# Optimization experiments

Measured on AMD Instinct MI355X. Metric: run time of the kernel, lower is better.

## Reference

```python
import jax, jax.numpy as jnp
import numpy as np

C = 256
INTER = C // 2


def _conv1x1(x, w, b):
    # x: [B,C,H,W], w: [O,C], b: [O] -> [B,O,H,W]
    return jnp.einsum('bchw,oc->bohw', x, w) + b[None, :, None, None]


def setup_inputs() -> dict:
    key = jax.random.key(0)
    ks = jax.random.split(key, 9)
    B, H, W = 4, 64, 64
    x = jax.random.normal(ks[0], (B, C, H, W), dtype=jnp.float32)
    s_in = 1.0 / np.sqrt(C)
    s_int = 1.0 / np.sqrt(INTER)
    return {
        'x': x,
        'w_g': jax.random.normal(ks[1], (INTER, C), jnp.float32) * s_in,
        'b_g': jax.random.normal(ks[2], (INTER,), jnp.float32) * 0.01,
        'w_theta': jax.random.normal(ks[3], (INTER, C), jnp.float32) * s_in,
        'b_theta': jax.random.normal(ks[4], (INTER,), jnp.float32) * 0.01,
        'w_phi': jax.random.normal(ks[5], (INTER, C), jnp.float32) * s_in,
        'b_phi': jax.random.normal(ks[6], (INTER,), jnp.float32) * 0.01,
        'w_W': jax.random.normal(ks[7], (C, INTER), jnp.float32) * s_int,
        'b_W': jax.random.normal(ks[8], (C,), jnp.float32) * 0.01,
    }


def reference(x, w_g, b_g, w_theta, b_theta, w_phi, b_phi, w_W, b_W):
    B, Cc, H, W = x.shape
    N = H * W
    # 1x1 conv projections -> flatten spatial to N
    g_x = _conv1x1(x, w_g, b_g).reshape(B, INTER, N).transpose(0, 2, 1)        # [B,N,I]
    theta_x = _conv1x1(x, w_theta, b_theta).reshape(B, INTER, N).transpose(0, 2, 1)  # [B,N,I]
    phi_x = _conv1x1(x, w_phi, b_phi).reshape(B, INTER, N)                     # [B,I,N]
    f = jnp.einsum('bni,bim->bnm', theta_x, phi_x)                             # [B,N,N]
    f_div_C = jax.nn.softmax(f, axis=-1)
    y = jnp.einsum('bnm,bmi->bni', f_div_C, g_x)                               # [B,N,I]
    y = y.transpose(0, 2, 1).reshape(B, INTER, H, W)
    W_y = _conv1x1(y, w_W, b_W)                                                # [B,C,H,W]
    return W_y + x
```

## Files before the change

### kernel.cpp

```cpp
#include <hip/hip_runtime.h>

typedef unsigned short ushort_t;
typedef unsigned int uint_t;
typedef _Float16 f16;
typedef __attribute__((ext_vector_type(8))) _Float16 f16x8;
typedef __attribute__((ext_vector_type(2))) _Float16 f16x2;
typedef __attribute__((ext_vector_type(4))) float f32x4;

#define B_ 4
#define C_ 256
#define I_ 128
#define N_ 4096
#define KVB 32
#define TOT_IT (N_ / KVB)
#define LOG2E 1.44269504f

#define W_F  0ull
#define TH_F 131072ull
#define PH_F 2228224ull
#define G3_F 4325376ull
#define YP_F 6422528ull

__device__ __forceinline__ float exp2_hw(float x) { return __builtin_amdgcn_exp2f(x); }
__device__ __forceinline__ float log2_hw(float x) { return __builtin_amdgcn_logf(x); }

__device__ __forceinline__ f16x2 pkrtz(float a, float b) {
    auto r = __builtin_amdgcn_cvt_pkrtz(a, b);
    f16x2 o;
    __builtin_memcpy(&o, &r, sizeof(o));
    return o;
}
__device__ __forceinline__ f32x4 mfma16h(f16x8 a, f16x8 b, f32x4 c) {
    return __builtin_amdgcn_mfma_f32_16x16x32_f16(a, b, c, 0, 0, 0);
}
__device__ __forceinline__ f32x4 zero4() { f32x4 z = {0.f, 0.f, 0.f, 0.f}; return z; }
__device__ __forceinline__ void gload_lds16(const void* g, void* lds) {
    __builtin_amdgcn_global_load_lds(
        (const __attribute__((address_space(1))) void*)g,
        (__attribute__((address_space(3))) void*)lds, 16, 0, 0);
}

__global__ __launch_bounds__(256) void k_convert_w(const float* wg, const float* wt,
                                                   const float* wp, const float* wW,
                                                   ushort_t* ws) {
    int idx = (blockIdx.x * 256 + threadIdx.x) * 16;
    const float* src;
    int off;
    if (idx < 32768)      { src = wg; off = idx; }
    else if (idx < 65536) { src = wt; off = idx - 32768; }
    else if (idx < 98304) { src = wp; off = idx - 65536; }
    else                  { src = wW; off = idx - 98304; }
    f16 o[16];
#pragma unroll
    for (int j = 0; j < 16; ++j) o[j] = (f16)src[off + j];
    f16* wd = (f16*)(ws + W_F);
    *(uint4*)&wd[idx]     = *(uint4*)&o[0];
    *(uint4*)&wd[idx + 8] = *(uint4*)&o[8];
}

__global__ __launch_bounds__(512) void k_projx(const float* x, const float* bg,
        const float* bth, const float* bph, ushort_t* ws) {
    __shared__ float t[64][65];
    __shared__ __align__(16) f16 xt[64][280];
    int b = blockIdx.y, n0 = blockIdx.x * 64;
    int tid = threadIdx.x;

    for (int q = 0; q < 4; ++q) {
        int c0 = q * 64;
#pragma unroll
        for (int p = 0; p < 2; ++p) {
            int row = p * 32 + (tid >> 4);
            int col4 = (tid & 15) * 4;
            float4 v = *(const float4*)(x + ((size_t)(b * C_ + c0 + row)) * N_ + n0 + col4);
            t[row][col4 + 0] = v.x; t[row][col4 + 1] = v.y;
            t[row][col4 + 2] = v.z; t[row][col4 + 3] = v.w;
        }
        __syncthreads();
        {
            int nl = tid & 63, cg = tid >> 6;
            f16 hv[8];
#pragma unroll
            for (int k = 0; k < 8; ++k) hv[k] = (f16)t[cg * 8 + k][nl];
            *(uint4*)&xt[nl][c0 + cg * 8] = *(uint4*)&hv[0];
        }
        __syncthreads();
    }

    int w = tid >> 6, l = tid & 63;
    int li = l & 15, lg = l >> 4;
    int wn = (w & 3) * 16;
    int ihb = (w >> 2) * 4;
    const f16* wf = (const f16*)(ws + W_F);

    f32x4 acc[3][4];
#pragma unroll
    for (int p = 0; p < 3; ++p)
#pragma unroll
        for (int t2 = 0; t2 < 4; ++t2) acc[p][t2] = zero4();

#pragma unroll 2
    for (int kb = 0; kb < 8; ++kb) {
        int kc = kb * 32 + 8 * lg;
        f16x8 ah = *(const f16x8*)&xt[wn + li][kc];
#pragma unroll
        for (int p = 0; p < 3; ++p)
#pragma unroll
            for (int t2 = 0; t2 < 4; ++t2) {
                f16x8 bw = *(const f16x8*)&wf[(size_t)p * 32768
                               + (size_t)((ihb + t2) * 16 + li) * C_ + kc];
                acc[p][t2] = mfma16h(ah, bw, acc[p][t2]);
            }
    }
    f16* g3p = (f16*)(ws + G3_F);
    f16* thp = (f16*)(ws + TH_F);
    f16* php = (f16*)(ws + PH_F);
#pragma unroll
    for (int p = 0; p < 3; ++p) {
        const float* bias = (p == 0) ? bg : (p == 1) ? bth : bph;
#pragma unroll
        for (int t2 = 0; t2 < 4; ++t2) {
            int i = (ihb + t2) * 16 + li;
            float bs = bias[i];
#pragma unroll
            for (int r = 0; r < 4; ++r) {
                int n = n0 + wn + 4 * lg + r;
                float v = acc[p][t2][r] + bs;
                if (p == 0) {
                    int tq = (n >> 2) & 3;
                    size_t gi = ((size_t)b * (N_ / 32) + (n >> 5)) * 4096
                              + (size_t)(tq * 128 + (i ^ (tq << 1))) * 8
                              + ((n >> 4) & 1) * 4 + (n & 3);
                    g3p[gi] = (f16)v;
                } else if (p == 1)
                    thp[((size_t)b * N_ + n) * I_ + i] = (f16)(v * LOG2E);
                else
                    php[((size_t)b * N_ + n) * I_ + i] = (f16)v;
            }
        }
    }
}

__global__ __launch_bounds__(256, 3) void k_attn(ushort_t* ws, float* lse, int splits) {
    __shared__ __align__(16) ushort_t smem[16384];
    int b = blockIdx.y, sp = blockIdx.z;
    int w = threadIdx.x >> 6, l = threadIdx.x & 63;
    int li = l & 15, lg = l >> 4;
    int q0 = blockIdx.x * 128 + w * 16;
    const f16* th = (const f16*)(ws + TH_F);
    const f16* ph = (const f16*)(ws + PH_F);
    const f16* g3 = (const f16*)(ws + G3_F);
    f16* yp = (f16*)(ws + YP_F) + (size_t)sp * 2097152ull;
    const f16* smf = (const f16*)smem;

    f16x8 qA[4], qB[4];
#pragma unroll
    for (int kb = 0; kb < 4; ++kb) {
        qA[kb] = *(const f16x8*)&th[((size_t)b * N_ + q0 + li) * I_ + kb * 32 + 8 * lg];
        qB[kb] = *(const f16x8*)&th[((size_t)b * N_ + q0 + 64 + li) * I_ + kb * 32 + 8 * lg];
    }

    int phOff[8];
#pragma unroll
    for (int kb = 0; kb < 4; ++kb) {
        int cc = ((kb * 4 + lg) ^ (li & 7)) * 8;
        phOff[kb * 2 + 0] = li * 128 + cc;
        phOff[kb * 2 + 1] = (16 + li) * 128 + cc;
    }
    int gBase = 8192 + (lg * 128 + (li ^ (lg << 1))) * 8;

    f32x4 yA[8], yB[8];
#pragma unroll
    for (int dt = 0; dt < 8; ++dt) { yA[dt] = zero4(); yB[dt] = zero4(); }
    float mA = -1e30f, lA = 0.f, mB = -1e30f, lB = 0.f;

    int beg = (sp * TOT_IT) / splits;
    int end = ((sp + 1) * TOT_IT) / splits;
    int nit = end - beg;
    int srow = l >> 4;
    const f16* srcP0 = ph + ((size_t)b * N_ + w * 8 + srow) * I_
                          + ((l & 15) ^ srow) * 8 + (size_t)beg * KVB * I_;
    const f16* srcP1 = ph + ((size_t)b * N_ + w * 8 + 4 + srow) * I_
                          + (((l & 15) ^ srow) ^ 4) * 8 + (size_t)beg * KVB * I_;
    const f16* srcG  = g3 + (size_t)b * (N_ / 32) * 4096 + w * 1024 + l * 8
                          + (size_t)beg * KVB * 128;

    gload_lds16(srcP0, smem + w * 1024);
    gload_lds16(srcP1, smem + w * 1024 + 512);
    gload_lds16(srcG,       smem + 8192 + w * 1024);
    gload_lds16(srcG + 512, smem + 8192 + w * 1024 + 512);
    srcP0 += 4096; srcP1 += 4096; srcG += 4096;
    __syncthreads();

#define ATTN_STEP(BUF, HASNEXT)                                                   \
    do {                                                                          \
        if (HASNEXT) {                                                            \
            gload_lds16(srcP0, smem + ((BUF) ^ 4096) + w * 1024);                 \
            gload_lds16(srcP1, smem + ((BUF) ^ 4096) + w * 1024 + 512);           \
            gload_lds16(srcG,       smem + 8192 + ((BUF) ^ 4096) + w * 1024);     \
            gload_lds16(srcG + 512, smem + 8192 + ((BUF) ^ 4096) + w * 1024 + 512);\
            srcP0 += 4096; srcP1 += 4096; srcG += 4096;                           \
        }                                                                         \
        f32x4 fA0 = zero4(), fA1 = zero4(), fB0 = zero4(), fB1 = zero4();         \
        __builtin_amdgcn_s_setprio(1);                                            \
        _Pragma("unroll")                                                         \
        for (int kb = 0; kb < 4; ++kb) {                                          \
            f16x8 a0 = *(const f16x8*)&smf[phOff[kb * 2 + 0] + (BUF)];            \
            f16x8 a1 = *(const f16x8*)&smf[phOff[kb * 2 + 1] + (BUF)];            \
            fA0 = mfma16h(a0, qA[kb], fA0);                                       \
            fB0 = mfma16h(a0, qB[kb], fB0);                                       \
            fA1 = mfma16h(a1, qA[kb], fA1);                                       \
            fB1 = mfma16h(a1, qB[kb], fB1);                                       \
        }                                                                         \
        __builtin_amdgcn_s_setprio(0);                                            \
        float tmA = fmaxf(fmaxf(fmaxf(fA0[0], fA0[1]), fmaxf(fA0[2], fA0[3])),    \
                          fmaxf(fmaxf(fA1[0], fA1[1]), fmaxf(fA1[2], fA1[3])));   \
        tmA = fmaxf(tmA, __shfl_xor(tmA, 16));                                    \
        tmA = fmaxf(tmA, __shfl_xor(tmA, 32));                                    \
        if (__ballot(tmA > mA + 11.0f)) {                                         \
            float mn = fmaxf(mA, tmA);                                            \
            float sc = exp2_hw(mA - mn);                                          \
            lA *= sc; mA = mn;                                                    \
            float s0 = __shfl(sc, 4 * lg + 0);                                    \
            float s1 = __shfl(sc, 4 * lg + 1);                                    \
            float s2 = __shfl(sc, 4 * lg + 2);                                    \
            float s3 = __shfl(sc, 4 * lg + 3);                                    \
            _Pragma("unroll")                                                     \
            for (int dt = 0; dt < 8; ++dt) {                                      \
                yA[dt][0] *= s0; yA[dt][1] *= s1;                                 \
                yA[dt][2] *= s2; yA[dt][3] *= s3;                                 \
            }                                                                     \
        }                                                                         \
        _Pragma("unroll")                                                         \
        for (int r = 0; r < 4; ++r) {                                             \
            fA0[r] = exp2_hw(fA0[r] - mA);                                        \
            fA1[r] = exp2_hw(fA1[r] - mA);                                        \
        }                                                                         \
        lA += ((fA0[0] + fA0[1]) + (fA0[2] + fA0[3]))                             \
            + ((fA1[0] + fA1[1]) + (fA1[2] + fA1[3]));                            \
        union PU { f16x2 h2[4]; f16x8 v; };                                       \
        PU pA, pB;                                                                \
        pA.h2[0] = pkrtz(fA0[0], fA0[1]); pA.h2[1] = pkrtz(fA0[2], fA0[3]);       \
        pA.h2[2] = pkrtz(fA1[0], fA1[1]); pA.h2[3] = pkrtz(fA1[2], fA1[3]);       \
        float tmB = fmaxf(fmaxf(fmaxf(fB0[0], fB0[1]), fmaxf(fB0[2], fB0[3])),    \
                          fmaxf(fmaxf(fB1[0], fB1[1]), fmaxf(fB1[2], fB1[3])));   \
        tmB = fmaxf(tmB, __shfl_xor(tmB, 16));                                    \
        tmB = fmaxf(tmB, __shfl_xor(tmB, 32));                                    \
        if (__ballot(tmB > mB + 11.0f)) {                                         \
            float mn = fmaxf(mB, tmB);                                            \
            float sc = exp2_hw(mB - mn);                                          \
            lB *= sc; mB = mn;                                                    \
            float s0 = __shfl(sc, 4 * lg + 0);                                    \
            float s1 = __shfl(sc, 4 * lg + 1);                                    \
            float s2 = __shfl(sc, 4 * lg + 2);                                    \
            float s3 = __shfl(sc, 4 * lg + 3);                                    \
            _Pragma("unroll")                                                     \
            for (int dt = 0; dt < 8; ++dt) {                                      \
                yB[dt][0] *= s0; yB[dt][1] *= s1;                                 \
                yB[dt][2] *= s2; yB[dt][3] *= s3;                                 \
            }                                                                     \
        }                                                                         \
        _Pragma("unroll")                                                         \
        for (int r = 0; r < 4; ++r) {                                             \
            fB0[r] = exp2_hw(fB0[r] - mB);                                        \
            fB1[r] = exp2_hw(fB1[r] - mB);                                        \
        }                                                                         \
        lB += ((fB0[0] + fB0[1]) + (fB0[2] + fB0[3]))                             \
            + ((fB1[0] + fB1[1]) + (fB1[2] + fB1[3]));                            \
        pB.h2[0] = pkrtz(fB0[0], fB0[1]); pB.h2[1] = pkrtz(fB0[2], fB0[3]);       \
        pB.h2[2] = pkrtz(fB1[0], fB1[1]); pB.h2[3] = pkrtz(fB1[2], fB1[3]);       \
        __builtin_amdgcn_s_setprio(1);                                            \
        _Pragma("unroll")                                                         \
        for (int dt = 0; dt < 8; ++dt) {                                          \
            f16x8 gv = *(const f16x8*)&smf[gBase + dt * 128 + (BUF)];             \
            yA[dt] = mfma16h(pA.v, gv, yA[dt]);                                   \
            yB[dt] = mfma16h(pB.v, gv, yB[dt]);                                   \
        }                                                                         \
        __builtin_amdgcn_s_setprio(0);                                            \
        __syncthreads();                                                          \
    } while (0)

    int it = 0;
    while (it + 2 <= nit) {
        ATTN_STEP(0, (it + 1 < nit));
        ATTN_STEP(4096, (it + 2 < nit));
        it += 2;
    }
    if (it < nit) ATTN_STEP(0, false);
#undef ATTN_STEP

    lA += __shfl_xor(lA, 16); lA += __shfl_xor(lA, 32);
    lB += __shfl_xor(lB, 16); lB += __shfl_xor(lB, 32);
    {
        float inv = 1.0f / lA;
        float i0 = __shfl(inv, 4 * lg + 0);
        float i1 = __shfl(inv, 4 * lg + 1);
        float i2 = __shfl(inv, 4 * lg + 2);
        float i3 = __shfl(inv, 4 * lg + 3);
#pragma unroll
        for (int dt = 0; dt < 8; ++dt) {
            size_t base = ((size_t)b * N_ + q0 + 4 * lg) * I_ + dt * 16 + li;
            yp[base]          = (f16)(yA[dt][0] * i0);
            yp[base + I_]     = (f16)(yA[dt][1] * i1);
            yp[base + 2 * I_] = (f16)(yA[dt][2] * i2);
            yp[base + 3 * I_] = (f16)(yA[dt][3] * i3);
        }
    }
    {
        float inv = 1.0f / lB;
        float i0 = __shfl(inv, 4 * lg + 0);
        float i1 = __shfl(inv, 4 * lg + 1);
        float i2 = __shfl(inv, 4 * lg + 2);
        float i3 = __shfl(inv, 4 * lg + 3);
#pragma unroll
        for (int dt = 0; dt < 8; ++dt) {
            size_t base = ((size_t)b * N_ + q0 + 64 + 4 * lg) * I_ + dt * 16 + li;
            yp[base]          = (f16)(yB[dt][0] * i0);
            yp[base + I_]     = (f16)(yB[dt][1] * i1);
            yp[base + 2 * I_] = (f16)(yB[dt][2] * i2);
            yp[base + 3 * I_] = (f16)(yB[dt][3] * i3);
        }
    }
    if (l < 16) {
        lse[((size_t)sp * B_ + b) * N_ + q0 + l]      = mA + log2_hw(lA);
        lse[((size_t)sp * B_ + b) * N_ + q0 + 64 + l] = mB + log2_hw(lB);
    }
}

__global__ __launch_bounds__(512) void k_out(const float* x, const float* bW,
        const ushort_t* ws, const float* lse, float* out, int splits) {
    __shared__ __align__(16) f16 ylds[64 * 136];
    int b = blockIdx.y, n0 = blockIdx.x * 64;
    int tid = threadIdx.x;
    {
        int nn = tid >> 3, ig = tid & 7;
        size_t lrow = (size_t)b * N_ + n0 + nn;
        float mx = -1e30f;
        for (int s = 0; s < splits; ++s)
            mx = fmaxf(mx, lse[(size_t)s * (B_ * N_) + lrow]);
        float sum = 0.f;
        for (int s = 0; s < splits; ++s)
            sum += exp2_hw(lse[(size_t)s * (B_ * N_) + lrow] - mx);
        float inv = 1.0f / sum;
        float acc[16];
#pragma unroll
        for (int j = 0; j < 16; ++j) acc[j] = 0.f;
        for (int s = 0; s < splits; ++s) {
            float wg = exp2_hw(lse[(size_t)s * (B_ * N_) + lrow] - mx) * inv;
            const f16* p = (const f16*)(ws + YP_F) + (size_t)s * 2097152ull
                         + lrow * I_ + ig * 16;
            f16x8 v0 = *(const f16x8*)p;
            f16x8 v1 = *(const f16x8*)(p + 8);
#pragma unroll
            for (int j = 0; j < 8; ++j) {
                acc[j]     += wg * (float)v0[j];
                acc[8 + j] += wg * (float)v1[j];
            }
        }
        f16 o[16];
#pragma unroll
        for (int j = 0; j < 16; ++j) o[j] = (f16)acc[j];
        *(uint4*)&ylds[nn * 136 + ig * 16]     = *(uint4*)&o[0];
        *(uint4*)&ylds[nn * 136 + ig * 16 + 8] = *(uint4*)&o[8];
    }
    __syncthreads();

    int w = tid >> 6, l = tid & 63;
    int li = l & 15, lg = l >> 4;
    int cw = (w >> 1) * 64, nh = (w & 1) * 32;
    const f16* wfp = (const f16*)(ws + W_F) + 98304;

    f32x4 acc2[4][2];
#pragma unroll
    for (int mm = 0; mm < 4; ++mm)
#pragma unroll
        for (int n = 0; n < 2; ++n) acc2[mm][n] = zero4();

#pragma unroll 2
    for (int kb = 0; kb < 4; ++kb) {
        int kc = kb * 32 + 8 * lg;
        f16x8 a[4], byv[2];
#pragma unroll
        for (int mm = 0; mm < 4; ++mm)
            a[mm] = *(const f16x8*)&wfp[(size_t)(cw + mm * 16 + li) * I_ + kc];
#pragma unroll
        for (int n = 0; n < 2; ++n)
            byv[n] = *(const f16x8*)&ylds[(nh + n * 16 + li) * 136 + kc];
#pragma unroll
        for (int mm = 0; mm < 4; ++mm)
#pragma unroll
            for (int n = 0; n < 2; ++n)
                acc2[mm][n] = mfma16h(a[mm], byv[n], acc2[mm][n]);
    }
#pragma unroll
    for (int mm = 0; mm < 4; ++mm)
#pragma unroll
        for (int n = 0; n < 2; ++n)
#pragma unroll
            for (int r = 0; r < 4; ++r) {
                int c = cw + mm * 16 + lg * 4 + r;
                int nn = n0 + nh + n * 16 + li;
                size_t xi = ((size_t)b * C_ + c) * N_ + nn;
                out[xi] = acc2[mm][n][r] + bW[c] + x[xi];
            }
}

extern "C" void kernel_launch(void* const* d_in, const int* in_sizes, int n_in,
                              void* d_out, int out_size, void* d_ws, size_t ws_size,
                              hipStream_t stream) {
    const float* x  = (const float*)d_in[0];
    const float* wg = (const float*)d_in[1];
    const float* bg = (const float*)d_in[2];
    const float* wt = (const float*)d_in[3];
    const float* bt = (const float*)d_in[4];
    const float* wp = (const float*)d_in[5];
    const float* bp = (const float*)d_in[6];
    const float* wW = (const float*)d_in[7];
    const float* bW = (const float*)d_in[8];
    ushort_t* ws = (ushort_t*)d_ws;
    float* out = (float*)d_out;

    int splits = (ws_size >= 46923776ull) ? 8
               : (ws_size >= 42663936ull) ? 7
               : (ws_size >= 38404096ull) ? 6 : 4;
    size_t lse_off = 2ull * (YP_F + (size_t)splits * 2097152ull);
    float* lse = (float*)((char*)d_ws + lse_off);

    k_convert_w<<<32, 256, 0, stream>>>(wg, wt, wp, wW, ws);
    k_projx<<<dim3(64, 4), 512, 0, stream>>>(x, bg, bt, bp, ws);
    k_attn<<<dim3(32, 4, splits), 256, 0, stream>>>(ws, lse, splits);
    k_out<<<dim3(64, 4), 512, 0, stream>>>(x, bW, ws, lse, out, splits);
}
```

Measured before the change: 104.7 us.

## Double block size of projection and output kernels, defer max shuffles in attention

```diff
diff --git a/kernel.cpp b/kernel.cpp
--- a/kernel.cpp
+++ b/kernel.cpp
@@ -58,7 +58,7 @@
     *(uint4*)&wd[idx + 8] = *(uint4*)&o[8];
 }
 
-__global__ __launch_bounds__(512) void k_projx(const float* x, const float* bg,
+__global__ __launch_bounds__(1024) void k_projx(const float* x, const float* bg,
         const float* bth, const float* bph, ushort_t* ws) {
     __shared__ float t[64][65];
     __shared__ __align__(16) f16 xt[64][280];
@@ -67,9 +67,8 @@
 
     for (int q = 0; q < 4; ++q) {
         int c0 = q * 64;
-#pragma unroll
-        for (int p = 0; p < 2; ++p) {
-            int row = p * 32 + (tid >> 4);
+        {
+            int row = tid >> 4;
             int col4 = (tid & 15) * 4;
             float4 v = *(const float4*)(x + ((size_t)(b * C_ + c0 + row)) * N_ + n0 + col4);
             t[row][col4 + 0] = v.x; t[row][col4 + 1] = v.y;
@@ -78,10 +77,10 @@
         __syncthreads();
         {
             int nl = tid & 63, cg = tid >> 6;
-            f16 hv[8];
-#pragma unroll
-            for (int k = 0; k < 8; ++k) hv[k] = (f16)t[cg * 8 + k][nl];
-            *(uint4*)&xt[nl][c0 + cg * 8] = *(uint4*)&hv[0];
+            f16 hv[4];
+#pragma unroll
+            for (int k = 0; k < 4; ++k) hv[k] = (f16)t[cg * 4 + k][nl];
+            *(uint2*)&xt[nl][c0 + cg * 4] = *(uint2*)&hv[0];
         }
         __syncthreads();
     }
@@ -89,53 +88,49 @@
     int w = tid >> 6, l = tid & 63;
     int li = l & 15, lg = l >> 4;
     int wn = (w & 3) * 16;
-    int ihb = (w >> 2) * 4;
+    int ip = w >> 2;
     const f16* wf = (const f16*)(ws + W_F);
 
-    f32x4 acc[3][4];
-#pragma unroll
-    for (int p = 0; p < 3; ++p)
-#pragma unroll
-        for (int t2 = 0; t2 < 4; ++t2) acc[p][t2] = zero4();
+    f32x4 acc[6];
+#pragma unroll
+    for (int t2 = 0; t2 < 6; ++t2) acc[t2] = zero4();
 
 #pragma unroll 2
     for (int kb = 0; kb < 8; ++kb) {
         int kc = kb * 32 + 8 * lg;
         f16x8 ah = *(const f16x8*)&xt[wn + li][kc];
 #pragma unroll
-        for (int p = 0; p < 3; ++p)
-#pragma unroll
-            for (int t2 = 0; t2 < 4; ++t2) {
-                f16x8 bw = *(const f16x8*)&wf[(size_t)p * 32768
-                               + (size_t)((ihb + t2) * 16 + li) * C_ + kc];
-                acc[p][t2] = mfma16h(ah, bw, acc[p][t2]);
-            }
+        for (int t2 = 0; t2 < 6; ++t2) {
+            int idx = ip * 6 + t2;
+            f16x8 bw = *(const f16x8*)&wf[(size_t)(idx >> 3) * 32768
+                           + (size_t)(((idx & 7) * 16 + li)) * C_ + kc];
+            acc[t2] = mfma16h(ah, bw, acc[t2]);
+        }
     }
     f16* g3p = (f16*)(ws + G3_F);
     f16* thp = (f16*)(ws + TH_F);
     f16* php = (f16*)(ws + PH_F);
 #pragma unroll
-    for (int p = 0; p < 3; ++p) {
+    for (int t2 = 0; t2 < 6; ++t2) {
+        int idx = ip * 6 + t2;
+        int p = idx >> 3;
+        int i = (idx & 7) * 16 + li;
         const float* bias = (p == 0) ? bg : (p == 1) ? bth : bph;
-#pragma unroll
-        for (int t2 = 0; t2 < 4; ++t2) {
-            int i = (ihb + t2) * 16 + li;
-            float bs = bias[i];
-#pragma unroll
-            for (int r = 0; r < 4; ++r) {
-                int n = n0 + wn + 4 * lg + r;
-                float v = acc[p][t2][r] + bs;
-                if (p == 0) {
-                    int tq = (n >> 2) & 3;
-                    size_t gi = ((size_t)b * (N_ / 32) + (n >> 5)) * 4096
-                              + (size_t)(tq * 128 + (i ^ (tq << 1))) * 8
-                              + ((n >> 4) & 1) * 4 + (n & 3);
-                    g3p[gi] = (f16)v;
-                } else if (p == 1)
-                    thp[((size_t)b * N_ + n) * I_ + i] = (f16)(v * LOG2E);
-                else
-                    php[((size_t)b * N_ + n) * I_ + i] = (f16)v;
-            }
+        float bs = bias[i];
+#pragma unroll
+        for (int r = 0; r < 4; ++r) {
+            int n = n0 + wn + 4 * lg + r;
+            float v = acc[t2][r] + bs;
+            if (p == 0) {
+                int tq = (n >> 2) & 3;
+                size_t gi = ((size_t)b * (N_ / 32) + (n >> 5)) * 4096
+                          + (size_t)(tq * 128 + (i ^ (tq << 1))) * 8
+                          + ((n >> 4) & 1) * 4 + (n & 3);
+                g3p[gi] = (f16)v;
+            } else if (p == 1)
+                thp[((size_t)b * N_ + n) * I_ + i] = (f16)(v * LOG2E);
+            else
+                php[((size_t)b * N_ + n) * I_ + i] = (f16)v;
         }
     }
 }
@@ -212,12 +207,12 @@
             fB1 = mfma16h(a1, qB[kb], fB1);                                       \
         }                                                                         \
         __builtin_amdgcn_s_setprio(0);                                            \
-        float tmA = fmaxf(fmaxf(fmaxf(fA0[0], fA0[1]), fmaxf(fA0[2], fA0[3])),    \
+        float gmA = fmaxf(fmaxf(fmaxf(fA0[0], fA0[1]), fmaxf(fA0[2], fA0[3])),    \
                           fmaxf(fmaxf(fA1[0], fA1[1]), fmaxf(fA1[2], fA1[3])));   \
-        tmA = fmaxf(tmA, __shfl_xor(tmA, 16));                                    \
-        tmA = fmaxf(tmA, __shfl_xor(tmA, 32));                                    \
-        if (__ballot(tmA > mA + 11.0f)) {                                         \
-            float mn = fmaxf(mA, tmA);                                            \
+        if (__ballot(gmA > mA + 11.0f)) {                                         \
+            float tm = fmaxf(gmA, __shfl_xor(gmA, 16));                           \
+            tm = fmaxf(tm, __shfl_xor(tm, 32));                                   \
+            float mn = fmaxf(mA, tm);                                             \
             float sc = exp2_hw(mA - mn);                                          \
             lA *= sc; mA = mn;                                                    \
             float s0 = __shfl(sc, 4 * lg + 0);                                    \
@@ -241,12 +236,12 @@
         PU pA, pB;                                                                \
         pA.h2[0] = pkrtz(fA0[0], fA0[1]); pA.h2[1] = pkrtz(fA0[2], fA0[3]);       \
         pA.h2[2] = pkrtz(fA1[0], fA1[1]); pA.h2[3] = pkrtz(fA1[2], fA1[3]);       \
-        float tmB = fmaxf(fmaxf(fmaxf(fB0[0], fB0[1]), fmaxf(fB0[2], fB0[3])),    \
+        float gmB = fmaxf(fmaxf(fmaxf(fB0[0], fB0[1]), fmaxf(fB0[2], fB0[3])),    \
                           fmaxf(fmaxf(fB1[0], fB1[1]), fmaxf(fB1[2], fB1[3])));   \
-        tmB = fmaxf(tmB, __shfl_xor(tmB, 16));                                    \
-        tmB = fmaxf(tmB, __shfl_xor(tmB, 32));                                    \
-        if (__ballot(tmB > mB + 11.0f)) {                                         \
-            float mn = fmaxf(mB, tmB);                                            \
+        if (__ballot(gmB > mB + 11.0f)) {                                         \
+            float tm = fmaxf(gmB, __shfl_xor(gmB, 16));                           \
+            tm = fmaxf(tm, __shfl_xor(tm, 32));                                   \
+            float mn = fmaxf(mB, tm);                                             \
             float sc = exp2_hw(mB - mn);                                          \
             lB *= sc; mB = mn;                                                    \
             float s0 = __shfl(sc, 4 * lg + 0);                                    \
@@ -326,13 +321,13 @@
     }
 }
 
-__global__ __launch_bounds__(512) void k_out(const float* x, const float* bW,
+__global__ __launch_bounds__(1024) void k_out(const float* x, const float* bW,
         const ushort_t* ws, const float* lse, float* out, int splits) {
     __shared__ __align__(16) f16 ylds[64 * 136];
     int b = blockIdx.y, n0 = blockIdx.x * 64;
     int tid = threadIdx.x;
     {
-        int nn = tid >> 3, ig = tid & 7;
+        int nn = tid >> 4, ig = tid & 15;
         size_t lrow = (size_t)b * N_ + n0 + nn;
         float mx = -1e30f;
         for (int s = 0; s < splits; ++s)
@@ -341,67 +336,52 @@
         for (int s = 0; s < splits; ++s)
             sum += exp2_hw(lse[(size_t)s * (B_ * N_) + lrow] - mx);
         float inv = 1.0f / sum;
-        float acc[16];
-#pragma unroll
-        for (int j = 0; j < 16; ++j) acc[j] = 0.f;
+        float acc[8];
+#pragma unroll
+        for (int j = 0; j < 8; ++j) acc[j] = 0.f;
         for (int s = 0; s < splits; ++s) {
             float wg = exp2_hw(lse[(size_t)s * (B_ * N_) + lrow] - mx) * inv;
             const f16* p = (const f16*)(ws + YP_F) + (size_t)s * 2097152ull
-                         + lrow * I_ + ig * 16;
+                         + lrow * I_ + ig * 8;
             f16x8 v0 = *(const f16x8*)p;
-            f16x8 v1 = *(const f16x8*)(p + 8);
-#pragma unroll
-            for (int j = 0; j < 8; ++j) {
-                acc[j]     += wg * (float)v0[j];
-                acc[8 + j] += wg * (float)v1[j];
-            }
-        }
-        f16 o[16];
-#pragma unroll
-        for (int j = 0; j < 16; ++j) o[j] = (f16)acc[j];
-        *(uint4*)&ylds[nn * 136 + ig * 16]     = *(uint4*)&o[0];
-        *(uint4*)&ylds[nn * 136 + ig * 16 + 8] = *(uint4*)&o[8];
+#pragma unroll
+            for (int j = 0; j < 8; ++j) acc[j] += wg * (float)v0[j];
+        }
+        f16 o[8];
+#pragma unroll
+        for (int j = 0; j < 8; ++j) o[j] = (f16)acc[j];
+        *(uint4*)&ylds[nn * 136 + ig * 8] = *(uint4*)&o[0];
     }
     __syncthreads();
 
     int w = tid >> 6, l = tid & 63;
     int li = l & 15, lg = l >> 4;
-    int cw = (w >> 1) * 64, nh = (w & 1) * 32;
+    int cw = (w >> 2) * 64, nsub = (w & 3) * 16;
     const f16* wfp = (const f16*)(ws + W_F) + 98304;
 
-    f32x4 acc2[4][2];
-#pragma unroll
-    for (int mm = 0; mm < 4; ++mm)
-#pragma unroll
-        for (int n = 0; n < 2; ++n) acc2[mm][n] = zero4();
+    f32x4 acc2[4];
+#pragma unroll
+    for (int mm = 0; mm < 4; ++mm) acc2[mm] = zero4();
 
 #pragma unroll 2
     for (int kb = 0; kb < 4; ++kb) {
         int kc = kb * 32 + 8 * lg;
-        f16x8 a[4], byv[2];
-#pragma unroll
-        for (int mm = 0; mm < 4; ++mm)
-            a[mm] = *(const f16x8*)&wfp[(size_t)(cw + mm * 16 + li) * I_ + kc];
-#pragma unroll
-        for (int n = 0; n < 2; ++n)
-            byv[n] = *(const f16x8*)&ylds[(nh + n * 16 + li) * 136 + kc];
-#pragma unroll
-        for (int mm = 0; mm < 4; ++mm)
-#pragma unroll
-            for (int n = 0; n < 2; ++n)
-                acc2[mm][n] = mfma16h(a[mm], byv[n], acc2[mm][n]);
+        f16x8 byv = *(const f16x8*)&ylds[(nsub + li) * 136 + kc];
+#pragma unroll
+        for (int mm = 0; mm < 4; ++mm) {
+            f16x8 a = *(const f16x8*)&wfp[(size_t)(cw + mm * 16 + li) * I_ + kc];
+            acc2[mm] = mfma16h(a, byv, acc2[mm]);
+        }
     }
 #pragma unroll
     for (int mm = 0; mm < 4; ++mm)
 #pragma unroll
-        for (int n = 0; n < 2; ++n)
-#pragma unroll
-            for (int r = 0; r < 4; ++r) {
-                int c = cw + mm * 16 + lg * 4 + r;
-                int nn = n0 + nh + n * 16 + li;
-                size_t xi = ((size_t)b * C_ + c) * N_ + nn;
-                out[xi] = acc2[mm][n][r] + bW[c] + x[xi];
-            }
+        for (int r = 0; r < 4; ++r) {
+            int c = cw + mm * 16 + lg * 4 + r;
+            int nn = n0 + nsub + li;
+            size_t xi = ((size_t)b * C_ + c) * N_ + nn;
+            out[xi] = acc2[mm][r] + bW[c] + x[xi];
+        }
 }
 
 extern "C" void kernel_launch(void* const* d_in, const int* in_sizes, int n_in,
@@ -426,7 +406,7 @@
     float* lse = (float*)((char*)d_ws + lse_off);
 
     k_convert_w<<<32, 256, 0, stream>>>(wg, wt, wp, wW, ws);
-    k_projx<<<dim3(64, 4), 512, 0, stream>>>(x, bg, bt, bp, ws);
+    k_projx<<<dim3(64, 4), 1024, 0, stream>>>(x, bg, bt, bp, ws);
     k_attn<<<dim3(32, 4, splits), 256, 0, stream>>>(ws, lse, splits);
-    k_out<<<dim3(64, 4), 512, 0, stream>>>(x, bW, ws, lse, out, splits);
-}
+    k_out<<<dim3(64, 4), 1024, 0, stream>>>(x, bW, ws, lse, out, splits);
+}
```

After: 107.3 us. 2.5% more time.
